# Kernel tuning notes

Measured on AMD Instinct MI355X. Metric: run time of the kernel, lower is better.

The kernel has to match this reference:

```python
import jax, jax.numpy as jnp
import numpy as np

# Tree: 64 leaves (16 feat -> 16 out), 8 mids (16 feat + 8*16 child = 144 -> 32 out),
# root (16 feat + 8*32 child = 272 -> 64 out), head -> 10 tasks. Eval-mode BatchNorm.
B = 16384
EPS = 1e-5


def setup_inputs() -> dict:
    key = jax.random.key(0)
    ks = jax.random.split(key, 24)
    rn = lambda k, s: jax.random.normal(k, s, dtype=jnp.float32)
    ru = lambda k, s: jax.random.uniform(k, s, dtype=jnp.float32)
    return {
        "x": rn(ks[0], (B, 1168)),
        # leaf layers (64 nodes, 16 -> 16)
        "Wl": rn(ks[1], (64, 16, 16)) * 0.1, "bl": rn(ks[2], (64, 16)) * 0.1,
        "gl": ru(ks[3], (64, 16)) + 0.5, "betal": rn(ks[4], (64, 16)) * 0.1,
        "ml": rn(ks[5], (64, 16)) * 0.1, "vl": ru(ks[6], (64, 16)) + 0.5,
        # mid layers (8 nodes, 144 -> 32)
        "Wm": rn(ks[7], (8, 144, 32)) * 0.1, "bm": rn(ks[8], (8, 32)) * 0.1,
        "gm": ru(ks[9], (8, 32)) + 0.5, "betam": rn(ks[10], (8, 32)) * 0.1,
        "mm": rn(ks[11], (8, 32)) * 0.1, "vm": ru(ks[12], (8, 32)) + 0.5,
        # root layer (272 -> 64)
        "Wr": rn(ks[13], (272, 64)) * 0.1, "br": rn(ks[14], (64,)) * 0.1,
        "gr": ru(ks[15], (64,)) + 0.5, "betar": rn(ks[16], (64,)) * 0.1,
        "mr": rn(ks[17], (64,)) * 0.1, "vr": ru(ks[18], (64,)) + 0.5,
        # root prediction head (64 -> 10 tasks)
        "Wh": rn(ks[19], (64, 10)) * 0.1, "bh": rn(ks[20], (10,)) * 0.1,
    }


def _bn(h, g, b, m, v):
    return (h - m) * jax.lax.rsqrt(v + EPS) * g + b


def reference(x, Wl, bl, gl, betal, ml, vl, Wm, bm, gm, betam, mm, vm,
              Wr, br, gr, betar, mr, vr, Wh, bh):
    n = x.shape[0]
    # leaves: gather own features (contiguous layout), Linear+BN+Tanh, batched over 64 nodes
    xl = x[:, :1024].reshape(n, 64, 16)
    hl = jnp.tanh(_bn(jnp.einsum('bli,lio->blo', xl, Wl) + bl, gl, betal, ml, vl))
    # mids: concat own features with 8 leaf-child outputs -> [n, 8, 144]
    xm = x[:, 1024:1152].reshape(n, 8, 16)
    mid_in = jnp.concatenate([xm, hl.reshape(n, 8, 128)], axis=-1)
    hm = jnp.tanh(_bn(jnp.einsum('bmi,mio->bmo', mid_in, Wm) + bm, gm, betam, mm, vm))
    # root: concat own features with 8 mid outputs -> [n, 272]
    root_in = jnp.concatenate([x[:, 1152:1168], hm.reshape(n, 256)], axis=-1)
    hr = jnp.tanh(_bn(root_in @ Wr + br, gr, betar, mr, vr))
    # root prediction head (eval-mode forward returns only root prediction)
    return hr @ Wh + bh
```

## Files before the change

### kernel.cpp

```cpp
#include <hip/hip_runtime.h>
#include <hip/hip_bf16.h>

typedef __attribute__((ext_vector_type(8))) short bf16x8;
typedef __attribute__((ext_vector_type(4))) float f32x4;

#define EPS 1e-5f
#define K2L 2.8853900817779268f

#define N_FRAG_BLOCKS 182
#define WSB_LEAF 0
#define WSB_MID  64
#define WSB_ROOT 144
#define WSB_HEAD 180
#define ST_SL 0
#define ST_TL 1024
#define ST_SM 2048
#define ST_TM 2304
#define ST_SR 2560
#define ST_TR 2624
#define WS_ST_BYTE_OFF (N_FRAG_BLOCKS * 1024)

#define XSW 1192

__device__ __forceinline__ unsigned short f2bf(float f) {
    unsigned u = __float_as_uint(f);
    unsigned r = u + 0x7fffu + ((u >> 16) & 1u);
    return (unsigned short)(r >> 16);
}

__device__ __forceinline__ unsigned pk2(float a, float b) {
    float2 f2; f2.x = a; f2.y = b;
    __hip_bfloat162 h = __float22bfloat162_rn(f2);
    union { __hip_bfloat162 h2; unsigned u; } cv; cv.h2 = h;
    return cv.u;
}

__device__ __forceinline__ float bn_act(float acc, float Sp, float Tp) {
    float e = exp2f(fmaf(acc, Sp, Tp));
    float r = __builtin_amdgcn_rcpf(e + 1.0f);
    return fmaf(-2.0f, r, 1.0f);
}

__global__ void ontology_prep(
    const float* __restrict__ Wl, const float* __restrict__ Wm,
    const float* __restrict__ Wr, const float* __restrict__ Wh,
    const float* __restrict__ bl, const float* __restrict__ gl,
    const float* __restrict__ betal, const float* __restrict__ ml,
    const float* __restrict__ vl,
    const float* __restrict__ bm, const float* __restrict__ gm,
    const float* __restrict__ betam, const float* __restrict__ mm,
    const float* __restrict__ vm,
    const float* __restrict__ br, const float* __restrict__ gr,
    const float* __restrict__ betar, const float* __restrict__ mr,
    const float* __restrict__ vr,
    unsigned short* __restrict__ wsFrag, float* __restrict__ wsST)
{
    const int tid = threadIdx.x;
    if (blockIdx.x < 46) {
        const int b = blockIdx.x * 4 + (tid >> 6);
        if (b >= N_FRAG_BLOCKS) return;
        const int t = tid & 63;
        const int row = t & 15, g = t >> 4;
        unsigned short vals[8];
        #pragma unroll
        for (int i = 0; i < 8; ++i) {
            const int k = g * 8 + i;
            float v = 0.f;
            if (b < 64) {
                const int l = b;
                if ((l & 1) == 0) { if (k < 16)  v = Wl[l * 256 + k * 16 + row]; }
                else              { if (k >= 16) v = Wl[l * 256 + (k - 16) * 16 + row]; }
            } else if (b < 144) {
                const int idx = b - 64, m = idx / 10, rem = idx % 10;
                const int tt = rem / 5, s = rem % 5;
                const int j = s * 32 + k;
                const int krow = (j < 128) ? (16 + j) : ((j < 144) ? (j - 128) : -1);
                if (krow >= 0) v = Wm[m * 4608 + krow * 32 + tt * 16 + row];
            } else if (b < 180) {
                const int idx = b - 144, tt = idx / 9, s = idx % 9;
                if (s == 0) { if (k < 16) v = Wr[k * 64 + tt * 16 + row]; }
                else { const int krow = 16 + (s - 1) * 32 + k;
                       v = Wr[krow * 64 + tt * 16 + row]; }
            } else {
                const int s = b - 180, krow = s * 32 + k;
                if (row < 10) v = Wh[krow * 10 + row];
            }
            vals[i] = f2bf(v);
        }
        #pragma unroll
        for (int i = 0; i < 8; ++i) wsFrag[b * 512 + t * 8 + i] = vals[i];
    } else {
        #pragma unroll
        for (int i = 0; i < 4; ++i) {
            const int id = tid + 256 * i;
            const float S = gl[id] * rsqrtf(vl[id] + EPS);
            wsST[ST_SL + id] = S * K2L;
            wsST[ST_TL + id] = ((bl[id] - ml[id]) * S + betal[id]) * K2L;
        }
        {
            const int id = tid;
            const float S = gm[id] * rsqrtf(vm[id] + EPS);
            wsST[ST_SM + id] = S * K2L;
            wsST[ST_TM + id] = ((bm[id] - mm[id]) * S + betam[id]) * K2L;
        }
        if (tid < 64) {
            const int id = tid;
            const float S = gr[id] * rsqrtf(vr[id] + EPS);
            wsST[ST_SR + id] = S * K2L;
            wsST[ST_TR + id] = ((br[id] - mr[id]) * S + betar[id]) * K2L;
        }
    }
}

__global__ __launch_bounds__(512, 8) void ontology_mfma(
    const float* __restrict__ x,
    const unsigned short* __restrict__ wsFrag,
    const float* __restrict__ wsST,
    const float* __restrict__ bh,
    float* __restrict__ out)
{
    __shared__ __align__(16) unsigned short xs[16 * XSW];

    const int tid  = threadIdx.x;
    const int w    = tid >> 6;
    const int lane = tid & 63;
    const int c    = lane & 15;
    const int g    = lane >> 4;
    const int rowbase = blockIdx.x * 16;

    const float* Sl = wsST + ST_SL; const float* Tl = wsST + ST_TL;
    const float* Sm = wsST + ST_SM; const float* Tm = wsST + ST_TM;
    const float* Sr = wsST + ST_SR; const float* Tr = wsST + ST_TR;

    {
        const float4* xt = (const float4*)(x + (size_t)rowbase * 1168);
        #pragma unroll
        for (int k = 0; k < 9; ++k) {
            const int idx4 = k * 512 + tid;
            float4 v = xt[idx4];
            const int f = idx4 * 4;
            const int row = f / 1168;
            const int col = f - row * 1168;
            uint2 p; p.x = pk2(v.x, v.y); p.y = pk2(v.z, v.w);
            *(uint2*)(xs + row * XSW + col) = p;
        }
        if (tid < 64) {
            const int idx4 = 4608 + tid;
            float4 v = xt[idx4];
            const int f = idx4 * 4;
            const int row = f / 1168;
            const int col = f - row * 1168;
            uint2 p; p.x = pk2(v.x, v.y); p.y = pk2(v.z, v.w);
            *(uint2*)(xs + row * XSW + col) = p;
        }
        if (tid < 64) {
            const int row = tid >> 2, seg = tid & 3;
            uint2 z; z.x = 0u; z.y = 0u;
            *(uint2*)(xs + row * XSW + 1168 + seg * 4) = z;
        }
    }
    __syncthreads();

    const int colbase = w * 128;
    #pragma unroll
    for (int p = 0; p < 4; ++p) {
        bf16x8 bfrag = *(const bf16x8*)(xs + c * XSW + colbase + p * 32 + g * 8);
        #pragma unroll
        for (int e = 0; e < 2; ++e) {
            const int l = 2 * p + e, leaf = w * 8 + l;
            bf16x8 afrag = *(const bf16x8*)(wsFrag + (WSB_LEAF + leaf) * 512 + lane * 8);
            f32x4 zz = {0.f,0.f,0.f,0.f};
            f32x4 acc = __builtin_amdgcn_mfma_f32_16x16x32_bf16(afrag, bfrag, zz, 0, 0, 0);
            const int po = leaf * 16 + 4 * g;
            float4 S = *(const float4*)(Sl + po);
            float4 T = *(const float4*)(Tl + po);
            uint2 pk;
            pk.x = pk2(bn_act(acc[0], S.x, T.x), bn_act(acc[1], S.y, T.y));
            pk.y = pk2(bn_act(acc[2], S.z, T.z), bn_act(acc[3], S.w, T.w));
            *(uint2*)(xs + c * XSW + colbase + l * 16 + 4 * g) = pk;
        }
    }

    {
        f32x4 acc0 = {0.f,0.f,0.f,0.f};
        f32x4 acc1 = {0.f,0.f,0.f,0.f};
        const unsigned short* fb = wsFrag + (WSB_MID + w * 10) * 512 + lane * 8;
        #pragma unroll
        for (int s = 0; s < 5; ++s) {
            const int cc = (s < 4) ? (colbase + s * 32) : (1024 + w * 16);
            bf16x8 bfrag = *(const bf16x8*)(xs + c * XSW + cc + g * 8);
            bf16x8 a0 = *(const bf16x8*)(fb + s * 512);
            bf16x8 a1 = *(const bf16x8*)(fb + (5 + s) * 512);
            acc0 = __builtin_amdgcn_mfma_f32_16x16x32_bf16(a0, bfrag, acc0, 0, 0, 0);
            acc1 = __builtin_amdgcn_mfma_f32_16x16x32_bf16(a1, bfrag, acc1, 0, 0, 0);
        }
        #pragma unroll
        for (int tt = 0; tt < 2; ++tt) {
            f32x4 acc = tt ? acc1 : acc0;
            const int po = w * 32 + tt * 16 + 4 * g;
            float4 S = *(const float4*)(Sm + po);
            float4 T = *(const float4*)(Tm + po);
            uint2 pk;
            pk.x = pk2(bn_act(acc[0], S.x, T.x), bn_act(acc[1], S.y, T.y));
            pk.y = pk2(bn_act(acc[2], S.z, T.z), bn_act(acc[3], S.w, T.w));
            *(uint2*)(xs + c * XSW + colbase + tt * 16 + 4 * g) = pk;
        }
    }
    __syncthreads();

    if (w < 4) {
        const unsigned short* fb = wsFrag + (WSB_ROOT + w * 9) * 512 + lane * 8;
        f32x4 acc = {0.f,0.f,0.f,0.f};
        {
            bf16x8 bfrag = *(const bf16x8*)(xs + c * XSW + 1152 + g * 8);
            bf16x8 a0 = *(const bf16x8*)fb;
            acc = __builtin_amdgcn_mfma_f32_16x16x32_bf16(a0, bfrag, acc, 0, 0, 0);
        }
        #pragma unroll
        for (int s = 1; s <= 8; ++s) {
            bf16x8 bfrag = *(const bf16x8*)(xs + c * XSW + (s - 1) * 128 + g * 8);
            bf16x8 a0 = *(const bf16x8*)(fb + s * 512);
            acc = __builtin_amdgcn_mfma_f32_16x16x32_bf16(a0, bfrag, acc, 0, 0, 0);
        }
        const int po = w * 16 + 4 * g;
        float4 S = *(const float4*)(Sr + po);
        float4 T = *(const float4*)(Tr + po);
        uint2 pk;
        pk.x = pk2(bn_act(acc[0], S.x, T.x), bn_act(acc[1], S.y, T.y));
        pk.y = pk2(bn_act(acc[2], S.z, T.z), bn_act(acc[3], S.w, T.w));
        *(uint2*)(xs + c * XSW + 32 + w * 16 + 4 * g) = pk;
    }
    __syncthreads();

    if (w == 0) {
        f32x4 acc = {0.f,0.f,0.f,0.f};
        #pragma unroll
        for (int s = 0; s < 2; ++s) {
            bf16x8 bfrag = *(const bf16x8*)(xs + c * XSW + 32 + s * 32 + g * 8);
            bf16x8 a0 = *(const bf16x8*)(wsFrag + (WSB_HEAD + s) * 512 + lane * 8);
            acc = __builtin_amdgcn_mfma_f32_16x16x32_bf16(a0, bfrag, acc, 0, 0, 0);
        }
        float* op = out + (size_t)(rowbase + c) * 10 + 4 * g;
        if (g < 2) {
            float2 o1 = {acc[0] + bh[4 * g],     acc[1] + bh[4 * g + 1]};
            float2 o2 = {acc[2] + bh[4 * g + 2], acc[3] + bh[4 * g + 3]};
            *(float2*)op = o1;
            *(float2*)(op + 2) = o2;
        } else if (g == 2) {
            float2 o1 = {acc[0] + bh[8], acc[1] + bh[9]};
            *(float2*)op = o1;
        }
    }
}

extern "C" void kernel_launch(void* const* d_in, const int* in_sizes, int n_in,
                              void* d_out, int out_size, void* d_ws, size_t ws_size,
                              hipStream_t stream) {
    const float* x     = (const float*)d_in[0];
    const float* Wl    = (const float*)d_in[1];
    const float* bl    = (const float*)d_in[2];
    const float* gl    = (const float*)d_in[3];
    const float* betal = (const float*)d_in[4];
    const float* ml    = (const float*)d_in[5];
    const float* vl    = (const float*)d_in[6];
    const float* Wm    = (const float*)d_in[7];
    const float* bm    = (const float*)d_in[8];
    const float* gm    = (const float*)d_in[9];
    const float* betam = (const float*)d_in[10];
    const float* mm    = (const float*)d_in[11];
    const float* vm    = (const float*)d_in[12];
    const float* Wr    = (const float*)d_in[13];
    const float* br    = (const float*)d_in[14];
    const float* gr    = (const float*)d_in[15];
    const float* betar = (const float*)d_in[16];
    const float* mr    = (const float*)d_in[17];
    const float* vr    = (const float*)d_in[18];
    const float* Wh    = (const float*)d_in[19];
    const float* bh    = (const float*)d_in[20];
    float* out = (float*)d_out;

    unsigned short* wsFrag = (unsigned short*)d_ws;
    float* wsST = (float*)((char*)d_ws + WS_ST_BYTE_OFF);

    ontology_prep<<<47, 256, 0, stream>>>(
        Wl, Wm, Wr, Wh, bl, gl, betal, ml, vl, bm, gm, betam, mm, vm,
        br, gr, betar, mr, vr, wsFrag, wsST);

    const int n = in_sizes[0] / 1168;
    ontology_mfma<<<n / 16, 512, 0, stream>>>(x, wsFrag, wsST, bh, out);
}
```

Baseline: 32.28 us.

## Process 32 rows per block, reusing weight fragments across two row tiles

Each block now handles 32 batch rows instead of 16. Every loaded weight fragment and BN scale/shift feeds two MFMAs, one per 16-row tile, which halves weight fragment global/L2 traffic per row and halves the block count. The cost is doubled LDS per block (about 76 KB) and more registers, with launch bounds lowered to 4 blocks per CU, so occupancy drops and fewer blocks (512) may leave the 256 CUs less evenly loaded.

```diff
diff --git a/kernel.cpp b/kernel.cpp
--- a/kernel.cpp
+++ b/kernel.cpp
@@ -112,21 +112,21 @@
     }
 }
 
-__global__ __launch_bounds__(512, 8) void ontology_mfma(
+__global__ __launch_bounds__(512, 4) void ontology_mfma(
     const float* __restrict__ x,
     const unsigned short* __restrict__ wsFrag,
     const float* __restrict__ wsST,
     const float* __restrict__ bh,
     float* __restrict__ out)
 {
-    __shared__ __align__(16) unsigned short xs[16 * XSW];
+    __shared__ __align__(16) unsigned short xs[32 * XSW];
 
     const int tid  = threadIdx.x;
     const int w    = tid >> 6;
     const int lane = tid & 63;
     const int c    = lane & 15;
     const int g    = lane >> 4;
-    const int rowbase = blockIdx.x * 16;
+    const int rowbase = blockIdx.x * 32;
 
     const float* Sl = wsST + ST_SL; const float* Tl = wsST + ST_TL;
     const float* Sm = wsST + ST_SM; const float* Tm = wsST + ST_TM;
@@ -135,7 +135,7 @@
     {
         const float4* xt = (const float4*)(x + (size_t)rowbase * 1168);
         #pragma unroll
-        for (int k = 0; k < 9; ++k) {
+        for (int k = 0; k < 18; ++k) {
             const int idx4 = k * 512 + tid;
             float4 v = xt[idx4];
             const int f = idx4 * 4;
@@ -144,8 +144,8 @@
             uint2 p; p.x = pk2(v.x, v.y); p.y = pk2(v.z, v.w);
             *(uint2*)(xs + row * XSW + col) = p;
         }
-        if (tid < 64) {
-            const int idx4 = 4608 + tid;
+        if (tid < 128) {
+            const int idx4 = 9216 + tid;
             float4 v = xt[idx4];
             const int f = idx4 * 4;
             const int row = f / 1168;
@@ -153,7 +153,7 @@
             uint2 p; p.x = pk2(v.x, v.y); p.y = pk2(v.z, v.w);
             *(uint2*)(xs + row * XSW + col) = p;
         }
-        if (tid < 64) {
+        if (tid < 128) {
             const int row = tid >> 2, seg = tid & 3;
             uint2 z; z.x = 0u; z.y = 0u;
             *(uint2*)(xs + row * XSW + 1168 + seg * 4) = z;
@@ -161,86 +161,109 @@
     }
     __syncthreads();
 
+    const int r0 = c;
+    const int r1 = 16 + c;
     const int colbase = w * 128;
+
     #pragma unroll
     for (int p = 0; p < 4; ++p) {
-        bf16x8 bfrag = *(const bf16x8*)(xs + c * XSW + colbase + p * 32 + g * 8);
+        bf16x8 bf0 = *(const bf16x8*)(xs + r0 * XSW + colbase + p * 32 + g * 8);
+        bf16x8 bf1 = *(const bf16x8*)(xs + r1 * XSW + colbase + p * 32 + g * 8);
         #pragma unroll
         for (int e = 0; e < 2; ++e) {
             const int l = 2 * p + e, leaf = w * 8 + l;
             bf16x8 afrag = *(const bf16x8*)(wsFrag + (WSB_LEAF + leaf) * 512 + lane * 8);
-            f32x4 zz = {0.f,0.f,0.f,0.f};
-            f32x4 acc = __builtin_amdgcn_mfma_f32_16x16x32_bf16(afrag, bfrag, zz, 0, 0, 0);
             const int po = leaf * 16 + 4 * g;
             float4 S = *(const float4*)(Sl + po);
             float4 T = *(const float4*)(Tl + po);
-            uint2 pk;
-            pk.x = pk2(bn_act(acc[0], S.x, T.x), bn_act(acc[1], S.y, T.y));
-            pk.y = pk2(bn_act(acc[2], S.z, T.z), bn_act(acc[3], S.w, T.w));
-            *(uint2*)(xs + c * XSW + colbase + l * 16 + 4 * g) = pk;
+            f32x4 zz = {0.f,0.f,0.f,0.f};
+            f32x4 a0 = __builtin_amdgcn_mfma_f32_16x16x32_bf16(afrag, bf0, zz, 0, 0, 0);
+            f32x4 a1 = __builtin_amdgcn_mfma_f32_16x16x32_bf16(afrag, bf1, zz, 0, 0, 0);
+            uint2 k0, k1;
+            k0.x = pk2(bn_act(a0[0], S.x, T.x), bn_act(a0[1], S.y, T.y));
+            k0.y = pk2(bn_act(a0[2], S.z, T.z), bn_act(a0[3], S.w, T.w));
+            k1.x = pk2(bn_act(a1[0], S.x, T.x), bn_act(a1[1], S.y, T.y));
+            k1.y = pk2(bn_act(a1[2], S.z, T.z), bn_act(a1[3], S.w, T.w));
+            *(uint2*)(xs + r0 * XSW + colbase + l * 16 + 4 * g) = k0;
+            *(uint2*)(xs + r1 * XSW + colbase + l * 16 + 4 * g) = k1;
         }
     }
 
     {
-        f32x4 acc0 = {0.f,0.f,0.f,0.f};
-        f32x4 acc1 = {0.f,0.f,0.f,0.f};
+        f32x4 c00 = {0.f,0.f,0.f,0.f}, c01 = {0.f,0.f,0.f,0.f};
+        f32x4 c10 = {0.f,0.f,0.f,0.f}, c11 = {0.f,0.f,0.f,0.f};
         const unsigned short* fb = wsFrag + (WSB_MID + w * 10) * 512 + lane * 8;
         #pragma unroll
         for (int s = 0; s < 5; ++s) {
             const int cc = (s < 4) ? (colbase + s * 32) : (1024 + w * 16);
-            bf16x8 bfrag = *(const bf16x8*)(xs + c * XSW + cc + g * 8);
+            bf16x8 bf0 = *(const bf16x8*)(xs + r0 * XSW + cc + g * 8);
+            bf16x8 bf1 = *(const bf16x8*)(xs + r1 * XSW + cc + g * 8);
             bf16x8 a0 = *(const bf16x8*)(fb + s * 512);
             bf16x8 a1 = *(const bf16x8*)(fb + (5 + s) * 512);
-            acc0 = __builtin_amdgcn_mfma_f32_16x16x32_bf16(a0, bfrag, acc0, 0, 0, 0);
-            acc1 = __builtin_amdgcn_mfma_f32_16x16x32_bf16(a1, bfrag, acc1, 0, 0, 0);
+            c00 = __builtin_amdgcn_mfma_f32_16x16x32_bf16(a0, bf0, c00, 0, 0, 0);
+            c01 = __builtin_amdgcn_mfma_f32_16x16x32_bf16(a1, bf0, c01, 0, 0, 0);
+            c10 = __builtin_amdgcn_mfma_f32_16x16x32_bf16(a0, bf1, c10, 0, 0, 0);
+            c11 = __builtin_amdgcn_mfma_f32_16x16x32_bf16(a1, bf1, c11, 0, 0, 0);
         }
         #pragma unroll
         for (int tt = 0; tt < 2; ++tt) {
-            f32x4 acc = tt ? acc1 : acc0;
             const int po = w * 32 + tt * 16 + 4 * g;
             float4 S = *(const float4*)(Sm + po);
             float4 T = *(const float4*)(Tm + po);
-            uint2 pk;
-            pk.x = pk2(bn_act(acc[0], S.x, T.x), bn_act(acc[1], S.y, T.y));
-            pk.y = pk2(bn_act(acc[2], S.z, T.z), bn_act(acc[3], S.w, T.w));
-            *(uint2*)(xs + c * XSW + colbase + tt * 16 + 4 * g) = pk;
+            f32x4 a0 = tt ? c01 : c00;
+            f32x4 a1 = tt ? c11 : c10;
+            uint2 k0, k1;
+            k0.x = pk2(bn_act(a0[0], S.x, T.x), bn_act(a0[1], S.y, T.y));
+            k0.y = pk2(bn_act(a0[2], S.z, T.z), bn_act(a0[3], S.w, T.w));
+            k1.x = pk2(bn_act(a1[0], S.x, T.x), bn_act(a1[1], S.y, T.y));
+            k1.y = pk2(bn_act(a1[2], S.z, T.z), bn_act(a1[3], S.w, T.w));
+            *(uint2*)(xs + r0 * XSW + colbase + tt * 16 + 4 * g) = k0;
+            *(uint2*)(xs + r1 * XSW + colbase + tt * 16 + 4 * g) = k1;
         }
     }
     __syncthreads();
 
     if (w < 4) {
         const unsigned short* fb = wsFrag + (WSB_ROOT + w * 9) * 512 + lane * 8;
-        f32x4 acc = {0.f,0.f,0.f,0.f};
+        f32x4 a0 = {0.f,0.f,0.f,0.f}, a1 = {0.f,0.f,0.f,0.f};
         {
-            bf16x8 bfrag = *(const bf16x8*)(xs + c * XSW + 1152 + g * 8);
-            bf16x8 a0 = *(const bf16x8*)fb;
-            acc = __builtin_amdgcn_mfma_f32_16x16x32_bf16(a0, bfrag, acc, 0, 0, 0);
+            bf16x8 bf0 = *(const bf16x8*)(xs + r0 * XSW + 1152 + g * 8);
+            bf16x8 bf1 = *(const bf16x8*)(xs + r1 * XSW + 1152 + g * 8);
+            bf16x8 af = *(const bf16x8*)fb;
+            a0 = __builtin_amdgcn_mfma_f32_16x16x32_bf16(af, bf0, a0, 0, 0, 0);
+            a1 = __builtin_amdgcn_mfma_f32_16x16x32_bf16(af, bf1, a1, 0, 0, 0);
         }
         #pragma unroll
         for (int s = 1; s <= 8; ++s) {
-            bf16x8 bfrag = *(const bf16x8*)(xs + c * XSW + (s - 1) * 128 + g * 8);
-            bf16x8 a0 = *(const bf16x8*)(fb + s * 512);
-            acc = __builtin_amdgcn_mfma_f32_16x16x32_bf16(a0, bfrag, acc, 0, 0, 0);
+            bf16x8 bf0 = *(const bf16x8*)(xs + r0 * XSW + (s - 1) * 128 + g * 8);
+            bf16x8 bf1 = *(const bf16x8*)(xs + r1 * XSW + (s - 1) * 128 + g * 8);
+            bf16x8 af = *(const bf16x8*)(fb + s * 512);
+            a0 = __builtin_amdgcn_mfma_f32_16x16x32_bf16(af, bf0, a0, 0, 0, 0);
+            a1 = __builtin_amdgcn_mfma_f32_16x16x32_bf16(af, bf1, a1, 0, 0, 0);
         }
         const int po = w * 16 + 4 * g;
         float4 S = *(const float4*)(Sr + po);
         float4 T = *(const float4*)(Tr + po);
-        uint2 pk;
-        pk.x = pk2(bn_act(acc[0], S.x, T.x), bn_act(acc[1], S.y, T.y));
-        pk.y = pk2(bn_act(acc[2], S.z, T.z), bn_act(acc[3], S.w, T.w));
-        *(uint2*)(xs + c * XSW + 32 + w * 16 + 4 * g) = pk;
+        uint2 k0, k1;
+        k0.x = pk2(bn_act(a0[0], S.x, T.x), bn_act(a0[1], S.y, T.y));
+        k0.y = pk2(bn_act(a0[2], S.z, T.z), bn_act(a0[3], S.w, T.w));
+        k1.x = pk2(bn_act(a1[0], S.x, T.x), bn_act(a1[1], S.y, T.y));
+        k1.y = pk2(bn_act(a1[2], S.z, T.z), bn_act(a1[3], S.w, T.w));
+        *(uint2*)(xs + r0 * XSW + 32 + w * 16 + 4 * g) = k0;
+        *(uint2*)(xs + r1 * XSW + 32 + w * 16 + 4 * g) = k1;
     }
     __syncthreads();
 
-    if (w == 0) {
+    if (w == 0 || w == 4) {
+        const int r = (w >> 2) * 16 + c;
         f32x4 acc = {0.f,0.f,0.f,0.f};
         #pragma unroll
         for (int s = 0; s < 2; ++s) {
-            bf16x8 bfrag = *(const bf16x8*)(xs + c * XSW + 32 + s * 32 + g * 8);
+            bf16x8 bfrag = *(const bf16x8*)(xs + r * XSW + 32 + s * 32 + g * 8);
             bf16x8 a0 = *(const bf16x8*)(wsFrag + (WSB_HEAD + s) * 512 + lane * 8);
             acc = __builtin_amdgcn_mfma_f32_16x16x32_bf16(a0, bfrag, acc, 0, 0, 0);
         }
-        float* op = out + (size_t)(rowbase + c) * 10 + 4 * g;
+        float* op = out + (size_t)(rowbase + r) * 10 + 4 * g;
         if (g < 2) {
             float2 o1 = {acc[0] + bh[4 * g],     acc[1] + bh[4 * g + 1]};
             float2 o2 = {acc[2] + bh[4 * g + 2], acc[3] + bh[4 * g + 3]};
@@ -287,5 +310,5 @@
         br, gr, betar, mr, vr, wsFrag, wsST);
 
     const int n = in_sizes[0] / 1168;
-    ontology_mfma<<<n / 16, 512, 0, stream>>>(x, wsFrag, wsST, bh, out);
-}
+    ontology_mfma<<<n / 32, 512, 0, stream>>>(x, wsFrag, wsST, bh, out);
+}
```

After: 31.95 us. Within noise of the previous version (-1.0%).
